# Kernel optimization log

Measured on AMD Instinct MI355X. Metric: run time of the kernel, lower is better.

## Reference

```python
import jax, jax.numpy as jnp
import numpy as np

N = 4096        # n_nodes; must equal HID due to the model's mean(dim=1)->classifier quirk
IN_DIM = 512
HID = 4096
E = 65536       # N * avg_degree(16)


def _lin(k, out_dim, in_dim):
    return jax.random.normal(k, (out_dim, in_dim), jnp.float32) * 0.02


def setup_inputs() -> dict:
    key = jax.random.key(0)
    ks = jax.random.split(key, 8)
    return {
        "x": jax.random.normal(ks[0], (N, IN_DIM), jnp.float32),
        "edge_index": jax.random.randint(ks[1], (2, E), 0, N, dtype=jnp.int32),
        "W_embed": _lin(ks[2], HID, IN_DIM),
        "b_embed": jnp.zeros((HID,), jnp.float32),
        "W1": _lin(ks[3], HID, HID),
        "b1": jnp.zeros((HID,), jnp.float32),
        "W2": _lin(ks[4], HID, HID),
        "b2": jnp.zeros((HID,), jnp.float32),
        "Wc1": _lin(ks[5], HID // 2, HID),
        "bc1": jnp.zeros((HID // 2,), jnp.float32),
        "Wc2": _lin(ks[6], 1, HID // 2),
        "bc2": jnp.zeros((1,), jnp.float32),
    }


def reference(x, edge_index, W_embed, b_embed, W1, b1, W2, b2, Wc1, bc1, Wc2, bc2):
    row, col = edge_index[0], edge_index[1]
    # embed: Linear(in_dim, hidden)
    h = x @ W_embed.T + b_embed                       # [N, HID]
    # two GNN layers: gather neighbors, scatter-add, linear + relu
    for W, b in ((W1, b1), (W2, b2)):
        aggr = jax.ops.segment_sum(h[col], row, num_segments=h.shape[0])  # [N, HID]
        h = jax.nn.relu(aggr @ W.T + b)
    # faithful to original: mean over feature dim -> [N] (N == HID)
    hm = jnp.mean(h, axis=1)                          # [HID]
    z = jax.nn.relu(hm @ Wc1.T + bc1)                 # [HID//2]
    out = (z @ Wc2.T + bc2).squeeze(-1)               # scalar
    return out
```

## Files before the change

### kernel.cpp

```cpp
#include <hip/hip_runtime.h>
#include <hip/hip_bf16.h>


#define N_NODES 4096
#define IN_DIM_ 512
#define HID_ 4096
#define NEDGE 65536

typedef float f32x4 __attribute__((ext_vector_type(4)));
typedef float f32x2 __attribute__((ext_vector_type(2)));
typedef unsigned short u16x8 __attribute__((ext_vector_type(8)));
typedef int i32x8 __attribute__((ext_vector_type(8)));

#define ACT_SCALE 8.0f
#define W_SCALE 256.0f
#define G_SCALE 8.0f
#define G_STORE_MUL (8.0f / 2048.0f)

__device__ __forceinline__ unsigned short f2bf(float f) {
  unsigned u = __float_as_uint(f);
  return (unsigned short)((u + 0x7fffu + ((u >> 16) & 1u)) >> 16);
}
__device__ __forceinline__ float bf2f(unsigned short h) {
  return __uint_as_float((unsigned)h << 16);
}
__device__ __forceinline__ unsigned char f2fp8(float f) {
  int w = __builtin_amdgcn_cvt_pk_fp8_f32(f, f, 0, false);
  return (unsigned char)(w & 0xff);
}
__device__ __forceinline__ void fp8x4_acc(int w, float* acc) {
  f32x2 lo = __builtin_amdgcn_cvt_pk_f32_fp8(w, false);
  f32x2 hi = __builtin_amdgcn_cvt_pk_f32_fp8(w, true);
  acc[0] += lo[0]; acc[1] += lo[1]; acc[2] += hi[0]; acc[3] += hi[1];
}

#define CVT_E0 ((long)N_NODES * IN_DIM_)
#define CVT_E1 (CVT_E0 + (long)HID_ * IN_DIM_)
#define CVT_E2 (CVT_E1 + (long)HID_ * HID_)
#define CVT_E3 (CVT_E2 + (long)HID_ * HID_)
__global__ __launch_bounds__(256) void cvt_all(
    const float* __restrict__ x, const float* __restrict__ We,
    const float* __restrict__ W1, const float* __restrict__ W2,
    unsigned char* __restrict__ xf8, unsigned char* __restrict__ wef8,
    unsigned char* __restrict__ w1f8, unsigned char* __restrict__ w2f8) {
  long i = ((long)blockIdx.x * 256 + threadIdx.x) * 8;
  const float* src; unsigned char* dst; float sc; long o;
  if (i < CVT_E0)      { src = x;  dst = xf8;  sc = ACT_SCALE; o = i; }
  else if (i < CVT_E1) { src = We; dst = wef8; sc = W_SCALE; o = i - CVT_E0; }
  else if (i < CVT_E2) { src = W1; dst = w1f8; sc = W_SCALE; o = i - CVT_E1; }
  else                 { src = W2; dst = w2f8; sc = W_SCALE; o = i - CVT_E2; }
  const float4 a = *(const float4*)(src + o);
  const float4 b = *(const float4*)(src + o + 4);
  int w0 = __builtin_amdgcn_cvt_pk_fp8_f32(a.x * sc, a.y * sc, 0, false);
  w0 = __builtin_amdgcn_cvt_pk_fp8_f32(a.z * sc, a.w * sc, w0, true);
  int w1 = __builtin_amdgcn_cvt_pk_fp8_f32(b.x * sc, b.y * sc, 0, false);
  w1 = __builtin_amdgcn_cvt_pk_fp8_f32(b.z * sc, b.w * sc, w1, true);
  *(int2*)(dst + o) = make_int2(w0, w1);
}

__global__ __launch_bounds__(256) void zero_i32(int* __restrict__ p, int n) {
  int i = blockIdx.x * 256 + threadIdx.x;
  if (i < n) p[i] = 0;
}

__global__ __launch_bounds__(256) void hist_rows(const int* __restrict__ row,
                                                 int* __restrict__ counts) {
  int e = blockIdx.x * 256 + threadIdx.x;
  if (e < NEDGE) atomicAdd(&counts[row[e]], 1);
}

__global__ __launch_bounds__(1024) void scan4096(const int* __restrict__ counts,
                                                 int* __restrict__ starts) {
  __shared__ int sa[1024], sb[1024];
  const int t = threadIdx.x;
  const int c0 = counts[t * 4], c1 = counts[t * 4 + 1],
            c2 = counts[t * 4 + 2], c3 = counts[t * 4 + 3];
  const int local = c0 + c1 + c2 + c3;
  sa[t] = local;
  __syncthreads();
  int* src = sa; int* dst = sb;
  for (int off = 1; off < 1024; off <<= 1) {
    int v = src[t];
    if (t >= off) v += src[t - off];
    dst[t] = v;
    __syncthreads();
    int* tmp = src; src = dst; dst = tmp;
  }
  const int excl = (t == 0) ? 0 : src[t - 1];
  starts[t * 4]     = excl;
  starts[t * 4 + 1] = excl + c0;
  starts[t * 4 + 2] = excl + c0 + c1;
  starts[t * 4 + 3] = excl + c0 + c1 + c2;
  if (t == 1023) starts[4096] = excl + local;
}

__global__ __launch_bounds__(256) void fill_adj(const int* __restrict__ row,
                                                const int* __restrict__ col,
                                                const int* __restrict__ starts,
                                                int* __restrict__ cursor,
                                                int* __restrict__ adj) {
  int e = blockIdx.x * 256 + threadIdx.x;
  if (e >= NEDGE) return;
  int r = row[e];
  int p = atomicAdd(&cursor[r], 1);
  adj[starts[r] + p] = col[e];
}

#define GLDS(gp, lp)                                                       \
  __builtin_amdgcn_global_load_lds(                                        \
      (const __attribute__((address_space(1))) void*)(gp),                 \
      (__attribute__((address_space(3))) void*)(lp), 16, 0, 0)

__global__ __launch_bounds__(512, 2) void gemm_mx(
    const unsigned char* __restrict__ A, const unsigned char* __restrict__ B,
    unsigned char* __restrict__ C, int N, int K,
    const float* __restrict__ bias, float mul) {
  __shared__ unsigned char lds[131072];
  const int t = threadIdx.x;
  const int w = blockIdx.x;
  const int xcd = w & 7, j = w >> 3;
  const int bm = ((xcd & 3) * 4 + (j & 3)) * 256;
  const int bn = ((xcd >> 2) * 8 + (j >> 2)) * 256;
  const int wave = t >> 6, lane = t & 63;
  const int wm = (wave >> 2) * 128, wn = (wave & 3) * 64;
  const int m16 = lane & 15, quad = lane >> 4;

  f32x4 acc[8][4] = {};

  const int rT = ((t >> 7) << 4) | (t & 15);
  const int kT = (((((t >> 4) & 3) << 1) | ((t >> 6) & 1))) << 4;
  const unsigned char* Ag = A + (size_t)(bm + rT) * K + kT;
  const unsigned char* Bg = B + (size_t)(bn + rT) * K + kT;
  const size_t rstep = (size_t)64 * K;
  unsigned char* Als = lds;
  unsigned char* Bls = lds + 65536;
  const int sd = t * 16;
  const int lane16 = lane * 16;

  const int KT = K >> 7;

#define STAGE_A(i, kb, dst) GLDS(Ag + (kb) + (size_t)(i) * rstep, (dst) + (i) * 8192 + sd)
#define STAGE_B(i, kb, dst) GLDS(Bg + (kb) + (size_t)(i) * rstep, (dst) + (i) * 8192 + sd)

#define LDFRAG(dst, base, fb)                                              \
  {                                                                        \
    const unsigned char* _p = (base) + (fb) * 2048 + lane16;               \
    const int4 _lo = *(const int4*)(_p);                                   \
    const int4 _hi = *(const int4*)(_p + 1024);                            \
    dst[0] = _lo.x; dst[1] = _lo.y; dst[2] = _lo.z; dst[3] = _lo.w;        \
    dst[4] = _hi.x; dst[5] = _hi.y; dst[6] = _hi.z; dst[7] = _hi.w;        \
  }

#define MFMA(r, c, afr, bfr)                                               \
  acc[r][c] = __builtin_amdgcn_mfma_scale_f32_16x16x128_f8f6f4(            \
      afr, bfr, acc[r][c], 0, 0, 0, 0x7f7f7f7f, 0, 0x7f7f7f7f)

  const int afb = (wave >> 2) * 8;
  const int bfb = (wave & 3) * 4;

  STAGE_A(0, 0, Als); STAGE_A(1, 0, Als); STAGE_A(2, 0, Als); STAGE_A(3, 0, Als);
  STAGE_B(0, 0, Bls); STAGE_B(1, 0, Bls); STAGE_B(2, 0, Bls); STAGE_B(3, 0, Bls);
  asm volatile("s_waitcnt vmcnt(0)" ::: "memory");
  __builtin_amdgcn_s_barrier();

  i32x8 af[4], bf01[2], bf23[2];

  for (int tt = 0; tt < KT; ++tt) {
    unsigned char* Ab = Als + (tt & 1) * 32768;
    unsigned char* Bb = Bls + (tt & 1) * 32768;
    unsigned char* An = Als + ((tt + 1) & 1) * 32768;
    unsigned char* Bn = Bls + ((tt + 1) & 1) * 32768;
    const int kbn = (tt + 1) << 7;
    const bool more = (tt + 1) < KT;

    LDFRAG(af[0], Ab, afb + 0);
    LDFRAG(af[1], Ab, afb + 1);
    LDFRAG(af[2], Ab, afb + 2);
    LDFRAG(af[3], Ab, afb + 3);
    LDFRAG(bf01[0], Bb, bfb + 0);
    LDFRAG(bf01[1], Bb, bfb + 1);
    LDFRAG(bf23[0], Bb, bfb + 2);
    LDFRAG(bf23[1], Bb, bfb + 3);
    if (more) {
      STAGE_A(0, kbn, An); STAGE_A(1, kbn, An);
      STAGE_A(2, kbn, An); STAGE_A(3, kbn, An);
    }
    __builtin_amdgcn_s_setprio(1);
    MFMA(0, 0, af[0], bf01[0]); MFMA(0, 1, af[0], bf01[1]);
    MFMA(1, 0, af[1], bf01[0]); MFMA(1, 1, af[1], bf01[1]);
    MFMA(2, 0, af[2], bf01[0]); MFMA(2, 1, af[2], bf01[1]);
    MFMA(3, 0, af[3], bf01[0]); MFMA(3, 1, af[3], bf01[1]);
    __builtin_amdgcn_s_setprio(0);
    if (more) {
      STAGE_B(0, kbn, Bn); STAGE_B(1, kbn, Bn);
      STAGE_B(2, kbn, Bn); STAGE_B(3, kbn, Bn);
    }
    __builtin_amdgcn_s_setprio(1);
    MFMA(0, 2, af[0], bf23[0]); MFMA(0, 3, af[0], bf23[1]);
    MFMA(1, 2, af[1], bf23[0]); MFMA(1, 3, af[1], bf23[1]);
    MFMA(2, 2, af[2], bf23[0]); MFMA(2, 3, af[2], bf23[1]);
    MFMA(3, 2, af[3], bf23[0]); MFMA(3, 3, af[3], bf23[1]);
    __builtin_amdgcn_s_setprio(0);
    LDFRAG(af[0], Ab, afb + 4);
    LDFRAG(af[1], Ab, afb + 5);
    LDFRAG(af[2], Ab, afb + 6);
    LDFRAG(af[3], Ab, afb + 7);
    __builtin_amdgcn_s_setprio(1);
    MFMA(4, 0, af[0], bf01[0]); MFMA(4, 1, af[0], bf01[1]);
    MFMA(5, 0, af[1], bf01[0]); MFMA(5, 1, af[1], bf01[1]);
    MFMA(6, 0, af[2], bf01[0]); MFMA(6, 1, af[2], bf01[1]);
    MFMA(7, 0, af[3], bf01[0]); MFMA(7, 1, af[3], bf01[1]);
    __builtin_amdgcn_s_setprio(0);
    __builtin_amdgcn_s_setprio(1);
    MFMA(4, 2, af[0], bf23[0]); MFMA(4, 3, af[0], bf23[1]);
    MFMA(5, 2, af[1], bf23[0]); MFMA(5, 3, af[1], bf23[1]);
    MFMA(6, 2, af[2], bf23[0]); MFMA(6, 3, af[2], bf23[1]);
    MFMA(7, 2, af[3], bf23[0]); MFMA(7, 3, af[3], bf23[1]);
    __builtin_amdgcn_s_setprio(0);
    if (more) {
      asm volatile("s_waitcnt vmcnt(0)" ::: "memory");
      __builtin_amdgcn_sched_barrier(0);
      __builtin_amdgcn_s_barrier();
    }
  }

#undef MFMA
#undef LDFRAG
#undef STAGE_A
#undef STAGE_B

#pragma unroll
  for (int r = 0; r < 8; ++r) {
#pragma unroll
    for (int c = 0; c < 4; ++c) {
      const int row0 = bm + wm + r * 16 + quad * 4;
      const int col = bn + wn + c * 16 + m16;
      const float bv = bias ? ACT_SCALE * bias[col] : 0.0f;
#pragma unroll
      for (int i = 0; i < 4; ++i) {
        C[(size_t)(row0 + i) * N + col] = f2fp8(acc[r][c][i] * mul + bv);
      }
    }
  }
}
#undef GLDS

__global__ __launch_bounds__(64) void aggr_f8out(
    const unsigned char* __restrict__ g, const int* __restrict__ starts,
    const int* __restrict__ adj, const float* __restrict__ bias,
    unsigned char* __restrict__ hout) {
  const int node = blockIdx.x >> 3;
  const int f0 = (blockIdx.x & 7) * 512 + threadIdx.x * 8;
  float acc[8] = {0, 0, 0, 0, 0, 0, 0, 0};
  const int s = starts[node], e = starts[node + 1];
  int j = s;
  for (; j + 4 <= e; j += 4) {
    const int c0 = adj[j], c1 = adj[j + 1], c2 = adj[j + 2], c3 = adj[j + 3];
    int2 v0 = *(const int2*)(g + (size_t)c0 * HID_ + f0);
    int2 v1 = *(const int2*)(g + (size_t)c1 * HID_ + f0);
    int2 v2 = *(const int2*)(g + (size_t)c2 * HID_ + f0);
    int2 v3 = *(const int2*)(g + (size_t)c3 * HID_ + f0);
    fp8x4_acc(v0.x, acc);     fp8x4_acc(v0.y, acc + 4);
    fp8x4_acc(v1.x, acc);     fp8x4_acc(v1.y, acc + 4);
    fp8x4_acc(v2.x, acc);     fp8x4_acc(v2.y, acc + 4);
    fp8x4_acc(v3.x, acc);     fp8x4_acc(v3.y, acc + 4);
  }
  for (; j < e; ++j) {
    int2 v = *(const int2*)(g + (size_t)adj[j] * HID_ + f0);
    fp8x4_acc(v.x, acc);      fp8x4_acc(v.y, acc + 4);
  }
  const float4 b0 = *(const float4*)(bias + f0);
  const float4 b1 = *(const float4*)(bias + f0 + 4);
  const float bb[8] = {b0.x, b0.y, b0.z, b0.w, b1.x, b1.y, b1.z, b1.w};
  float v[8];
#pragma unroll
  for (int i = 0; i < 8; ++i)
    v[i] = ACT_SCALE * fmaxf(acc[i] * (1.0f / G_SCALE) + bb[i], 0.0f);
  int w0 = __builtin_amdgcn_cvt_pk_fp8_f32(v[0], v[1], 0, false);
  w0 = __builtin_amdgcn_cvt_pk_fp8_f32(v[2], v[3], w0, true);
  int w1 = __builtin_amdgcn_cvt_pk_fp8_f32(v[4], v[5], 0, false);
  w1 = __builtin_amdgcn_cvt_pk_fp8_f32(v[6], v[7], w1, true);
  *(int2*)(hout + (size_t)node * HID_ + f0) = make_int2(w0, w1);
}

__global__ __launch_bounds__(64) void aggr_mean(
    const unsigned char* __restrict__ g, const int* __restrict__ starts,
    const int* __restrict__ adj, const float* __restrict__ bias,
    float* __restrict__ hm) {
  const int node = blockIdx.x >> 3;
  const int f0 = (blockIdx.x & 7) * 512 + threadIdx.x * 8;
  float acc[8] = {0, 0, 0, 0, 0, 0, 0, 0};
  const int s = starts[node], e = starts[node + 1];
  int j = s;
  for (; j + 4 <= e; j += 4) {
    const int c0 = adj[j], c1 = adj[j + 1], c2 = adj[j + 2], c3 = adj[j + 3];
    int2 v0 = *(const int2*)(g + (size_t)c0 * HID_ + f0);
    int2 v1 = *(const int2*)(g + (size_t)c1 * HID_ + f0);
    int2 v2 = *(const int2*)(g + (size_t)c2 * HID_ + f0);
    int2 v3 = *(const int2*)(g + (size_t)c3 * HID_ + f0);
    fp8x4_acc(v0.x, acc);     fp8x4_acc(v0.y, acc + 4);
    fp8x4_acc(v1.x, acc);     fp8x4_acc(v1.y, acc + 4);
    fp8x4_acc(v2.x, acc);     fp8x4_acc(v2.y, acc + 4);
    fp8x4_acc(v3.x, acc);     fp8x4_acc(v3.y, acc + 4);
  }
  for (; j < e; ++j) {
    int2 v = *(const int2*)(g + (size_t)adj[j] * HID_ + f0);
    fp8x4_acc(v.x, acc);      fp8x4_acc(v.y, acc + 4);
  }
  const float4 b0 = *(const float4*)(bias + f0);
  const float4 b1 = *(const float4*)(bias + f0 + 4);
  const float bb[8] = {b0.x, b0.y, b0.z, b0.w, b1.x, b1.y, b1.z, b1.w};
  float local = 0.f;
#pragma unroll
  for (int i = 0; i < 8; ++i)
    local += fmaxf(acc[i] * (1.0f / G_SCALE) + bb[i], 0.0f);
  for (int off = 32; off > 0; off >>= 1) local += __shfl_down(local, off);
  if (threadIdx.x == 0)
    atomicAdd(&hm[node], local * (1.0f / (float)HID_));
}

__global__ __launch_bounds__(256) void clf1(const float* __restrict__ Wc1,
                                            const float* __restrict__ bc1,
                                            const float* __restrict__ hm,
                                            float* __restrict__ z) {
  const int wave = threadIdx.x >> 6, lane = threadIdx.x & 63;
  const int j = blockIdx.x * 4 + wave;
  const float* w = Wc1 + (size_t)j * HID_;
  float s = 0.f;
  for (int i = lane; i < HID_; i += 64) s += w[i] * hm[i];
  for (int off = 32; off > 0; off >>= 1) s += __shfl_down(s, off);
  if (lane == 0) z[j] = fmaxf(s + bc1[j], 0.0f);
}

__global__ __launch_bounds__(256) void clf2(const float* __restrict__ Wc2,
                                            const float* __restrict__ bc2,
                                            const float* __restrict__ z,
                                            float* __restrict__ out) {
  const int t = threadIdx.x;
  float s = 0.f;
  for (int i = t; i < HID_ / 2; i += 256) s += z[i] * Wc2[i];
  for (int off = 32; off > 0; off >>= 1) s += __shfl_down(s, off);
  __shared__ float ws[4];
  if ((t & 63) == 0) ws[t >> 6] = s;
  __syncthreads();
  if (t == 0) out[0] = ws[0] + ws[1] + ws[2] + ws[3] + bc2[0];
}

extern "C" void kernel_launch(void* const* d_in, const int* in_sizes, int n_in,
                              void* d_out, int out_size, void* d_ws, size_t ws_size,
                              hipStream_t stream) {
  (void)in_sizes; (void)n_in; (void)out_size; (void)ws_size;
  const float* x       = (const float*)d_in[0];
  const int*   edge    = (const int*)d_in[1];
  const int*   row     = edge;
  const int*   col     = edge + NEDGE;
  const float* W_embed = (const float*)d_in[2];
  const float* b_embed = (const float*)d_in[3];
  const float* W1      = (const float*)d_in[4];
  const float* b1      = (const float*)d_in[5];
  const float* W2      = (const float*)d_in[6];
  const float* b2      = (const float*)d_in[7];
  const float* Wc1     = (const float*)d_in[8];
  const float* bc1     = (const float*)d_in[9];
  const float* Wc2     = (const float*)d_in[10];
  const float* bc2     = (const float*)d_in[11];
  float* out = (float*)d_out;

  char* ws = (char*)d_ws;
  size_t off = 0;
  auto alloc = [&](size_t bytes) {
    char* p = ws + off;
    off += (bytes + 255) & ~(size_t)255;
    return p;
  };
  unsigned char*  xf8  = (unsigned char*)alloc((size_t)N_NODES * IN_DIM_);
  unsigned char*  wef8 = (unsigned char*)alloc((size_t)HID_ * IN_DIM_);
  unsigned char*  w1f8 = (unsigned char*)alloc((size_t)HID_ * HID_);
  unsigned char*  w2f8 = (unsigned char*)alloc((size_t)HID_ * HID_);
  unsigned char*  h0f8 = (unsigned char*)alloc((size_t)N_NODES * HID_);
  unsigned char*  h1f8 = (unsigned char*)alloc((size_t)N_NODES * HID_);
  unsigned char*  g    = (unsigned char*)alloc((size_t)N_NODES * HID_);
  int*   counts = (int*)alloc(N_NODES * 4);
  int*   cursor = (int*)alloc(N_NODES * 4);
  float* hm     = (float*)alloc(N_NODES * 4);
  int*   starts = (int*)alloc((N_NODES + 1) * 4);
  int*   adj    = (int*)alloc(NEDGE * 4);
  float* z      = (float*)alloc((HID_ / 2) * 4);

  zero_i32<<<48, 256, 0, stream>>>(counts, 3 * N_NODES);
  hist_rows<<<NEDGE / 256, 256, 0, stream>>>(row, counts);
  scan4096<<<1, 1024, 0, stream>>>(counts, starts);
  fill_adj<<<NEDGE / 256, 256, 0, stream>>>(row, col, starts, cursor, adj);

  cvt_all<<<(int)(CVT_E3 / 2048), 256, 0, stream>>>(x, W_embed, W1, W2,
                                                    xf8, wef8, w1f8, w2f8);

  gemm_mx<<<256, 512, 0, stream>>>(xf8, wef8, h0f8, HID_, IN_DIM_,
                                   b_embed, G_STORE_MUL);
  gemm_mx<<<256, 512, 0, stream>>>(h0f8, w1f8, g, HID_, HID_,
                                   nullptr, G_STORE_MUL);
  aggr_f8out<<<N_NODES * 8, 64, 0, stream>>>(g, starts, adj, b1, h1f8);
  gemm_mx<<<256, 512, 0, stream>>>(h1f8, w2f8, g, HID_, HID_,
                                   nullptr, G_STORE_MUL);
  aggr_mean<<<N_NODES * 8, 64, 0, stream>>>(g, starts, adj, b2, hm);
  clf1<<<(HID_ / 2) / 4, 256, 0, stream>>>(Wc1, bc1, hm, z);
  clf2<<<1, 256, 0, stream>>>(Wc2, bc2, z, out);
}
```

Measured before the change: 503.5 us.

## Pre-swizzle fp8 operands into tile-contiguous layout for GEMM loads

```diff
diff --git a/kernel.cpp b/kernel.cpp
--- a/kernel.cpp
+++ b/kernel.cpp
@@ -34,28 +34,42 @@
   acc[0] += lo[0]; acc[1] += lo[1]; acc[2] += hi[0]; acc[3] += hi[1];
 }
 
-#define CVT_E0 ((long)N_NODES * IN_DIM_)
-#define CVT_E1 (CVT_E0 + (long)HID_ * IN_DIM_)
-#define CVT_E2 (CVT_E1 + (long)HID_ * HID_)
-#define CVT_E3 (CVT_E2 + (long)HID_ * HID_)
+#define SL_X  131072L
+#define SL_WE 262144L
+#define SL_W1 1310720L
+#define SL_W2 2359296L
 __global__ __launch_bounds__(256) void cvt_all(
     const float* __restrict__ x, const float* __restrict__ We,
     const float* __restrict__ W1, const float* __restrict__ W2,
     unsigned char* __restrict__ xf8, unsigned char* __restrict__ wef8,
     unsigned char* __restrict__ w1f8, unsigned char* __restrict__ w2f8) {
-  long i = ((long)blockIdx.x * 256 + threadIdx.x) * 8;
-  const float* src; unsigned char* dst; float sc; long o;
-  if (i < CVT_E0)      { src = x;  dst = xf8;  sc = ACT_SCALE; o = i; }
-  else if (i < CVT_E1) { src = We; dst = wef8; sc = W_SCALE; o = i - CVT_E0; }
-  else if (i < CVT_E2) { src = W1; dst = w1f8; sc = W_SCALE; o = i - CVT_E1; }
-  else                 { src = W2; dst = w2f8; sc = W_SCALE; o = i - CVT_E2; }
-  const float4 a = *(const float4*)(src + o);
-  const float4 b = *(const float4*)(src + o + 4);
+  long S = (long)blockIdx.x * 256 + threadIdx.x;
+  const float* src; unsigned char* dst; float sc; long So; int K, ktb;
+  if (S < SL_X)       { src = x;  dst = xf8;  sc = ACT_SCALE; So = S;         K = 512;  ktb = 2; }
+  else if (S < SL_WE) { src = We; dst = wef8; sc = W_SCALE;   So = S - SL_X;  K = 512;  ktb = 2; }
+  else if (S < SL_W1) { src = W1; dst = w1f8; sc = W_SCALE;   So = S - SL_WE; K = 4096; ktb = 5; }
+  else                { src = W2; dst = w2f8; sc = W_SCALE;   So = S - SL_W1; K = 4096; ktb = 5; }
+  const long region = So >> 7;
+  const int rem = (int)(So & 127);
+  const int h = (rem >> 6) & 1, q = (rem >> 4) & 3, m = rem & 15;
+  const long R16 = region >> ktb;
+  const int kt = (int)(region & ((1 << ktb) - 1));
+  const long row = R16 * 16 + m;
+  const int k0 = kt * 128 + q * 32 + h * 16;
+  const float* p = src + row * K + k0;
+  const float4 a = *(const float4*)(p);
+  const float4 b = *(const float4*)(p + 4);
+  const float4 c = *(const float4*)(p + 8);
+  const float4 d = *(const float4*)(p + 12);
   int w0 = __builtin_amdgcn_cvt_pk_fp8_f32(a.x * sc, a.y * sc, 0, false);
   w0 = __builtin_amdgcn_cvt_pk_fp8_f32(a.z * sc, a.w * sc, w0, true);
   int w1 = __builtin_amdgcn_cvt_pk_fp8_f32(b.x * sc, b.y * sc, 0, false);
   w1 = __builtin_amdgcn_cvt_pk_fp8_f32(b.z * sc, b.w * sc, w1, true);
-  *(int2*)(dst + o) = make_int2(w0, w1);
+  int w2 = __builtin_amdgcn_cvt_pk_fp8_f32(c.x * sc, c.y * sc, 0, false);
+  w2 = __builtin_amdgcn_cvt_pk_fp8_f32(c.z * sc, c.w * sc, w2, true);
+  int w3 = __builtin_amdgcn_cvt_pk_fp8_f32(d.x * sc, d.y * sc, 0, false);
+  w3 = __builtin_amdgcn_cvt_pk_fp8_f32(d.z * sc, d.w * sc, w3, true);
+  *(int4*)(dst + So * 16) = make_int4(w0, w1, w2, w3);
 }
 
 __global__ __launch_bounds__(256) void zero_i32(int* __restrict__ p, int n) {
@@ -114,7 +128,7 @@
 __global__ __launch_bounds__(512, 2) void gemm_mx(
     const unsigned char* __restrict__ A, const unsigned char* __restrict__ B,
     unsigned char* __restrict__ C, int N, int K,
-    const float* __restrict__ bias, float mul) {
+    const float* __restrict__ bias, float mul, int permC) {
   __shared__ unsigned char lds[131072];
   const int t = threadIdx.x;
   const int w = blockIdx.x;
@@ -127,20 +141,17 @@
 
   f32x4 acc[8][4] = {};
 
-  const int rT = ((t >> 7) << 4) | (t & 15);
-  const int kT = (((((t >> 4) & 3) << 1) | ((t >> 6) & 1))) << 4;
-  const unsigned char* Ag = A + (size_t)(bm + rT) * K + kT;
-  const unsigned char* Bg = B + (size_t)(bn + rT) * K + kT;
-  const size_t rstep = (size_t)64 * K;
+  const int KT = K >> 7;
+  const unsigned char* Ag = A + ((size_t)(bm >> 4) + (t >> 7)) * KT * 2048 + (t & 127) * 16;
+  const unsigned char* Bg = B + ((size_t)(bn >> 4) + (t >> 7)) * KT * 2048 + (t & 127) * 16;
+  const size_t istep = (size_t)8192 * KT;
   unsigned char* Als = lds;
   unsigned char* Bls = lds + 65536;
   const int sd = t * 16;
   const int lane16 = lane * 16;
 
-  const int KT = K >> 7;
-
-#define STAGE_A(i, kb, dst) GLDS(Ag + (kb) + (size_t)(i) * rstep, (dst) + (i) * 8192 + sd)
-#define STAGE_B(i, kb, dst) GLDS(Bg + (kb) + (size_t)(i) * rstep, (dst) + (i) * 8192 + sd)
+#define STAGE_A(i, kb, dst) GLDS(Ag + (kb) + (size_t)(i) * istep, (dst) + (i) * 8192 + sd)
+#define STAGE_B(i, kb, dst) GLDS(Bg + (kb) + (size_t)(i) * istep, (dst) + (i) * 8192 + sd)
 
 #define LDFRAG(dst, base, fb)                                              \
   {                                                                        \
@@ -170,7 +181,7 @@
     unsigned char* Bb = Bls + (tt & 1) * 32768;
     unsigned char* An = Als + ((tt + 1) & 1) * 32768;
     unsigned char* Bn = Bls + ((tt + 1) & 1) * 32768;
-    const int kbn = (tt + 1) << 7;
+    const int kbn = (tt + 1) * 2048;
     const bool more = (tt + 1) < KT;
 
     LDFRAG(af[0], Ab, afb + 0);
@@ -229,16 +240,36 @@
 #undef STAGE_A
 #undef STAGE_B
 
-#pragma unroll
-  for (int r = 0; r < 8; ++r) {
-#pragma unroll
-    for (int c = 0; c < 4; ++c) {
-      const int row0 = bm + wm + r * 16 + quad * 4;
-      const int col = bn + wn + c * 16 + m16;
-      const float bv = bias ? ACT_SCALE * bias[col] : 0.0f;
-#pragma unroll
-      for (int i = 0; i < 4; ++i) {
-        C[(size_t)(row0 + i) * N + col] = f2fp8(acc[r][c][i] * mul + bv);
+  if (permC) {
+    const int KTN = N >> 7;
+#pragma unroll
+    for (int r = 0; r < 8; ++r) {
+#pragma unroll
+      for (int c = 0; c < 4; ++c) {
+        const int rb = ((bm + wm) >> 4) + r;
+        const int colb = bn + wn + c * 16;
+        const float bv = bias ? ACT_SCALE * bias[colb + m16] : 0.0f;
+        const size_t base = ((size_t)rb * KTN + (colb >> 7)) * 2048
+                          + (((colb >> 4) & 1) << 10)
+                          + (((colb >> 5) & 3) << 8) + m16;
+#pragma unroll
+        for (int i = 0; i < 4; ++i) {
+          C[base + (quad * 4 + i) * 16] = f2fp8(acc[r][c][i] * mul + bv);
+        }
+      }
+    }
+  } else {
+#pragma unroll
+    for (int r = 0; r < 8; ++r) {
+#pragma unroll
+      for (int c = 0; c < 4; ++c) {
+        const int row0 = bm + wm + r * 16 + quad * 4;
+        const int col = bn + wn + c * 16 + m16;
+        const float bv = bias ? ACT_SCALE * bias[col] : 0.0f;
+#pragma unroll
+        for (int i = 0; i < 4; ++i) {
+          C[(size_t)(row0 + i) * N + col] = f2fp8(acc[r][c][i] * mul + bv);
+        }
       }
     }
   }
@@ -280,7 +311,10 @@
   w0 = __builtin_amdgcn_cvt_pk_fp8_f32(v[2], v[3], w0, true);
   int w1 = __builtin_amdgcn_cvt_pk_fp8_f32(v[4], v[5], 0, false);
   w1 = __builtin_amdgcn_cvt_pk_fp8_f32(v[6], v[7], w1, true);
-  *(int2*)(hout + (size_t)node * HID_ + f0) = make_int2(w0, w1);
+  const size_t oaddr = ((size_t)(node >> 4) * 32 + (f0 >> 7)) * 2048
+                     + (((f0 >> 4) & 1) << 10)
+                     + (((f0 >> 5) & 3) << 8) + ((node & 15) << 4) + (f0 & 15);
+  *(int2*)(hout + oaddr) = make_int2(w0, w1);
 }
 
 __global__ __launch_bounds__(64) void aggr_mean(
@@ -392,16 +426,16 @@
   scan4096<<<1, 1024, 0, stream>>>(counts, starts);
   fill_adj<<<NEDGE / 256, 256, 0, stream>>>(row, col, starts, cursor, adj);
 
-  cvt_all<<<(int)(CVT_E3 / 2048), 256, 0, stream>>>(x, W_embed, W1, W2,
-                                                    xf8, wef8, w1f8, w2f8);
+  cvt_all<<<(int)(SL_W2 / 256), 256, 0, stream>>>(x, W_embed, W1, W2,
+                                                  xf8, wef8, w1f8, w2f8);
 
   gemm_mx<<<256, 512, 0, stream>>>(xf8, wef8, h0f8, HID_, IN_DIM_,
-                                   b_embed, G_STORE_MUL);
+                                   b_embed, G_STORE_MUL, 1);
   gemm_mx<<<256, 512, 0, stream>>>(h0f8, w1f8, g, HID_, HID_,
-                                   nullptr, G_STORE_MUL);
+                                   nullptr, G_STORE_MUL, 0);
   aggr_f8out<<<N_NODES * 8, 64, 0, stream>>>(g, starts, adj, b1, h1f8);
   gemm_mx<<<256, 512, 0, stream>>>(h1f8, w2f8, g, HID_, HID_,
-                                   nullptr, G_STORE_MUL);
+                                   nullptr, G_STORE_MUL, 0);
   aggr_mean<<<N_NODES * 8, 64, 0, stream>>>(g, starts, adj, b2, hm);
   clf1<<<(HID_ / 2) / 4, 256, 0, stream>>>(Wc1, bc1, hm, z);
   clf2<<<1, 256, 0, stream>>>(Wc2, bc2, z, out);
```

Measured after the change: 433.5 us (median of 2 runs). 13.9% less time.
